# Kernel optimization log

Hardware: AMD Instinct MI355X
Metric: run time of the kernel (lower is better)

The kernel has to match this reference:

```python
import jax, jax.numpy as jnp
import numpy as np

B, C_IN, N, K = 8, 64, 16384, 9
C_OUT = 128


def setup_inputs() -> dict:
    key = jax.random.key(0)
    k1, k2, k3, k4 = jax.random.split(key, 4)
    x = jax.random.normal(k1, (B, C_IN, N, 1), dtype=jnp.float32)
    edge_index = jax.random.randint(k2, (2, B, N, K), 0, N, dtype=jnp.int32)
    # 1x1 Conv2d weight/bias of the MLP2dLayer: in = 2*C_IN, out = C_OUT
    W = jax.random.normal(k3, (C_OUT, 2 * C_IN), dtype=jnp.float32) * (1.0 / np.sqrt(2 * C_IN))
    b = jax.random.normal(k4, (C_OUT,), dtype=jnp.float32) * 0.01
    return {"x": x, "edge_index": edge_index, "W": W, "b": b}


def reference(x, edge_index, W, b):
    # x: [B, C, N, 1]; edge_index: [2, B, N, K] (edge_index[0] = neighbor idx)
    Bb, C, Nn, _ = x.shape
    idx = edge_index[0]                      # [B, N, K]
    x3 = x[..., 0]                           # [B, C, N]
    # batched_index_select: gather neighbor features x_j [B, C, N, K]
    idx_flat = idx.reshape(Bb, 1, Nn * idx.shape[-1])
    idx_flat = jnp.broadcast_to(idx_flat, (Bb, C, idx_flat.shape[-1]))
    x_j = jnp.take_along_axis(x3, idx_flat, axis=2).reshape(Bb, C, Nn, -1)
    # max-relative aggregation over neighbors (keepdim)
    aggr = jnp.max(x_j - x3[..., None], axis=-1, keepdims=True)  # [B, C, N, 1]
    feat = jnp.concatenate([x, aggr], axis=1)                    # [B, 2C, N, 1]
    # 1x1 conv MLP + ReLU (norm=None)
    out = jnp.einsum('oc,bcnk->bonk', W, feat) + b[None, :, None, None]
    return jax.nn.relu(out)
```

## Files before the change

kernel.cpp:

```cpp
#include <hip/hip_runtime.h>
#include <float.h>

#define NB 8
#define CIN 64
#define NPTS 16384
#define KNB 9
#define COUT 128
#define TN 64
#define FPAD 65
#define LDB 136

typedef float f32x4 __attribute__((ext_vector_type(4)));
typedef __bf16 bf16x8 __attribute__((ext_vector_type(8)));

__device__ __forceinline__ ushort f2bf_rne(float f) {
    unsigned u = __float_as_uint(f);
    unsigned r = u + 0x7FFFu + ((u >> 16) & 1u);
    return (ushort)(r >> 16);
}
__device__ __forceinline__ float bf2f(ushort h) {
    return __uint_as_float(((unsigned)h) << 16);
}

__global__ __launch_bounds__(256) void prep_kernel(const float* __restrict__ x,
                                                   const float* __restrict__ W,
                                                   float* __restrict__ xt,
                                                   ushort* __restrict__ Whi,
                                                   ushort* __restrict__ Wlo) {
    int blk = blockIdx.x;
    if (blk == NB * (NPTS / 64)) {
        for (int i = threadIdx.x; i < COUT * 2 * CIN; i += 256) {
            float w = W[i];
            ushort h = f2bf_rne(w);
            Whi[i] = h;
            Wlo[i] = f2bf_rne(w - bf2f(h));
        }
        return;
    }
    __shared__ float t[64][65];
    int b   = blk >> 8;
    int n0  = (blk & 255) << 6;
    int tid = threadIdx.x;
    int hi  = tid >> 4;
    int lo  = tid & 15;
    const float* xb = x + (size_t)b * CIN * NPTS;

#pragma unroll
    for (int cc = 0; cc < 4; ++cc) {
        int c = cc * 16 + hi;
        int n = lo * 4;
        float4 v = *reinterpret_cast<const float4*>(&xb[(size_t)c * NPTS + n0 + n]);
        t[c][n + 0] = v.x; t[c][n + 1] = v.y; t[c][n + 2] = v.z; t[c][n + 3] = v.w;
    }
    __syncthreads();

    float* xtb = xt + (size_t)b * NPTS * 64;
#pragma unroll
    for (int it = 0; it < 4; ++it) {
        int n  = it * 16 + hi;
        int c4 = lo * 4;
        float4 v;
        v.x = t[c4 + 0][n]; v.y = t[c4 + 1][n]; v.z = t[c4 + 2][n]; v.w = t[c4 + 3][n];
        *reinterpret_cast<float4*>(&xtb[(size_t)(n0 + n) * 64 + c4]) = v;
    }
}

__global__ __launch_bounds__(256, 4) void mrconv_main(const int*    __restrict__ eidx,
                                                      const ushort* __restrict__ Whi,
                                                      const ushort* __restrict__ Wlo,
                                                      const float*  __restrict__ bias,
                                                      const float*  __restrict__ xt,
                                                      float*        __restrict__ out) {
    __shared__ __align__(16) ushort fhi[TN][LDB];
    __shared__ __align__(16) ushort flo[TN][LDB];

    int blk  = blockIdx.x;
    int b    = blk & 7;
    int tile = blk >> 3;
    int n0   = tile * TN;

    int tid  = threadIdx.x;
    int lane = tid & 63;
    int wid  = __builtin_amdgcn_readfirstlane(tid >> 6);
    int l16  = lane & 15;
    int lh   = lane >> 4;

    const float* xtb = xt + (size_t)b * NPTS * 64;
    const int*   eb  = eidx + ((size_t)b * NPTS + n0) * KNB;

#pragma unroll 2
    for (int i = 0; i < 16; ++i) {
        int n = wid * 16 + i;
        float xc = xtb[(size_t)(n0 + n) * 64 + lane];
        ushort xh = f2bf_rne(xc);
        fhi[n][lane] = xh;
        flo[n][lane] = f2bf_rne(xc - bf2f(xh));
        const int* ep = eb + n * KNB;
        float m = -FLT_MAX;
#pragma unroll
        for (int k = 0; k < KNB; ++k) {
            int j = ep[k];
            float xj = xtb[(size_t)j * 64 + lane];
            m = fmaxf(m, xj - xc);
        }
        ushort mh = f2bf_rne(m);
        fhi[n][CIN + lane] = mh;
        flo[n][CIN + lane] = f2bf_rne(m - bf2f(mh));
    }

    bf16x8 ahi[2][4], alo[2][4];
#pragma unroll
    for (int mt = 0; mt < 2; ++mt)
#pragma unroll
        for (int kb = 0; kb < 4; ++kb) {
            int off = (wid * 32 + mt * 16 + l16) * (2 * CIN) + kb * 32 + lh * 8;
            ahi[mt][kb] = *reinterpret_cast<const bf16x8*>(Whi + off);
            alo[mt][kb] = *reinterpret_cast<const bf16x8*>(Wlo + off);
        }

    __syncthreads();

    f32x4 acc[2][4];
#pragma unroll
    for (int mt = 0; mt < 2; ++mt)
#pragma unroll
        for (int nt = 0; nt < 4; ++nt)
            acc[mt][nt] = (f32x4){0.f, 0.f, 0.f, 0.f};

#pragma unroll
    for (int nt = 0; nt < 4; ++nt) {
#pragma unroll
        for (int kb = 0; kb < 4; ++kb) {
            const bf16x8 bhi = *reinterpret_cast<const bf16x8*>(&fhi[nt * 16 + l16][kb * 32 + lh * 8]);
            const bf16x8 blo = *reinterpret_cast<const bf16x8*>(&flo[nt * 16 + l16][kb * 32 + lh * 8]);
#pragma unroll
            for (int mt = 0; mt < 2; ++mt) {
                acc[mt][nt] = __builtin_amdgcn_mfma_f32_16x16x32_bf16(ahi[mt][kb], bhi, acc[mt][nt], 0, 0, 0);
                acc[mt][nt] = __builtin_amdgcn_mfma_f32_16x16x32_bf16(ahi[mt][kb], blo, acc[mt][nt], 0, 0, 0);
                acc[mt][nt] = __builtin_amdgcn_mfma_f32_16x16x32_bf16(alo[mt][kb], bhi, acc[mt][nt], 0, 0, 0);
            }
        }
    }

    float* ob = out + (size_t)b * COUT * NPTS + n0;
#pragma unroll
    for (int mt = 0; mt < 2; ++mt)
#pragma unroll
        for (int nt = 0; nt < 4; ++nt)
#pragma unroll
            for (int r = 0; r < 4; ++r) {
                int o = wid * 32 + mt * 16 + lh * 4 + r;
                int n = nt * 16 + l16;
                float v = acc[mt][nt][r] + bias[o];
                ob[(size_t)o * NPTS + n] = fmaxf(v, 0.f);
            }
}

__global__ __launch_bounds__(256) void mrconv_direct(const float* __restrict__ x,
                                                     const int*   __restrict__ eidx,
                                                     const float* __restrict__ W,
                                                     const float* __restrict__ bias,
                                                     float* __restrict__ out) {
    __shared__ float feat[2 * CIN][FPAD];

    int blk  = blockIdx.x;
    int b    = blk & 7;
    int tile = blk >> 3;
    int n0   = tile * TN;

    int tid  = threadIdx.x;
    int lane = tid & 63;
    int wid  = __builtin_amdgcn_readfirstlane(tid >> 6);

    const float* xb = x + (size_t)b * CIN * NPTS;
    const int*   eb = eidx + ((size_t)b * NPTS + n0) * KNB;

#pragma unroll
    for (int i = 0; i < 16; ++i) {
        int c = wid * 16 + i;
        feat[c][lane] = xb[(size_t)c * NPTS + n0 + lane];
    }
    __syncthreads();

    const float* xc_row = xb + (size_t)lane * NPTS;
#pragma unroll 2
    for (int i = 0; i < 16; ++i) {
        int n = i * 4 + wid;
        float xc = feat[lane][n];
        const int* ep = eb + n * KNB;
        float m = -FLT_MAX;
#pragma unroll
        for (int k = 0; k < KNB; ++k) {
            int j = ep[k];
            m = fmaxf(m, xc_row[j] - xc);
        }
        feat[CIN + lane][n] = m;
    }
    __syncthreads();

    int o_base = wid * 32;
    float acc[32];
#pragma unroll
    for (int oo = 0; oo < 32; ++oo) acc[oo] = 0.f;

    for (int c = 0; c < 2 * CIN; ++c) {
        float f = feat[c][lane];
#pragma unroll
        for (int oo = 0; oo < 32; ++oo)
            acc[oo] = fmaf(W[(o_base + oo) * (2 * CIN) + c], f, acc[oo]);
    }

    float* ob = out + (size_t)b * COUT * NPTS + n0;
#pragma unroll
    for (int oo = 0; oo < 32; ++oo) {
        int o = o_base + oo;
        float v = acc[oo] + bias[o];
        ob[(size_t)o * NPTS + lane] = fmaxf(v, 0.f);
    }
}

extern "C" void kernel_launch(void* const* d_in, const int* in_sizes, int n_in,
                              void* d_out, int out_size, void* d_ws, size_t ws_size,
                              hipStream_t stream) {
    const float* x    = (const float*)d_in[0];
    const int*   eidx = (const int*)  d_in[1];
    const float* W    = (const float*)d_in[2];
    const float* bias = (const float*)d_in[3];
    float*       out  = (float*)d_out;

    const size_t xt_elems = (size_t)NB * NPTS * 64;
    const size_t need = xt_elems * sizeof(float) + (size_t)2 * 2 * CIN * COUT * sizeof(ushort);

    if (ws_size >= need) {
        float*  xt  = (float*)d_ws;
        ushort* Whi = (ushort*)(xt + xt_elems);
        ushort* Wlo = Whi + (size_t)2 * CIN * COUT;

        dim3 blkA(256), grdA(NB * (NPTS / 64) + 1);
        hipLaunchKernelGGL(prep_kernel, grdA, blkA, 0, stream, x, W, xt, Whi, Wlo);

        dim3 blkB(256), grdB(NB * (NPTS / TN));
        hipLaunchKernelGGL(mrconv_main, grdB, blkB, 0, stream, eidx, Whi, Wlo, bias, xt, out);
    } else {
        dim3 blkB(256), grdB(NB * (NPTS / TN));
        hipLaunchKernelGGL(mrconv_direct, grdB, blkB, 0, stream, x, eidx, W, bias, out);
    }
}
```

Baseline: 144.1 us.

## Swizzle feature LDS layout, prefetch center features, raise occupancy hint to 5

Replaces the padded LDS feature tiles with unpadded 128-wide rows using an XOR swizzle on 8-element chunks, so the bf16x8 MFMA operand reads avoid bank conflicts and the tiles use less LDS. All 16 center-point features are loaded into registers up front and written to LDS before the gather loop, which is now unrolled by 4 so more neighbor loads can be in flight. The launch bound goes from 4 to 5 blocks per SM. The tradeoff is higher register pressure under a tighter occupancy bound, which could cause spills.

```diff
diff --git a/kernel.cpp b/kernel.cpp
--- a/kernel.cpp
+++ b/kernel.cpp
@@ -8,7 +8,6 @@
 #define COUT 128
 #define TN 64
 #define FPAD 65
-#define LDB 136
 
 typedef float f32x4 __attribute__((ext_vector_type(4)));
 typedef __bf16 bf16x8 __attribute__((ext_vector_type(8)));
@@ -20,6 +19,10 @@
 }
 __device__ __forceinline__ float bf2f(ushort h) {
     return __uint_as_float(((unsigned)h) << 16);
+}
+
+__device__ __forceinline__ int swz16(int row, int us) {
+    return row * 128 + ((((us >> 3) ^ (row & 15)) << 3) | (us & 7));
 }
 
 __global__ __launch_bounds__(256) void prep_kernel(const float* __restrict__ x,
@@ -65,14 +68,14 @@
     }
 }
 
-__global__ __launch_bounds__(256, 4) void mrconv_main(const int*    __restrict__ eidx,
+__global__ __launch_bounds__(256, 5) void mrconv_main(const int*    __restrict__ eidx,
                                                       const ushort* __restrict__ Whi,
                                                       const ushort* __restrict__ Wlo,
                                                       const float*  __restrict__ bias,
                                                       const float*  __restrict__ xt,
                                                       float*        __restrict__ out) {
-    __shared__ __align__(16) ushort fhi[TN][LDB];
-    __shared__ __align__(16) ushort flo[TN][LDB];
+    __shared__ __align__(16) ushort fhi[TN * 128];
+    __shared__ __align__(16) ushort flo[TN * 128];
 
     int blk  = blockIdx.x;
     int b    = blk & 7;
@@ -88,13 +91,23 @@
     const float* xtb = xt + (size_t)b * NPTS * 64;
     const int*   eb  = eidx + ((size_t)b * NPTS + n0) * KNB;
 
-#pragma unroll 2
+    float xcv[16];
+#pragma unroll
+    for (int i = 0; i < 16; ++i)
+        xcv[i] = xtb[(size_t)(n0 + wid * 16 + i) * 64 + lane];
+
+#pragma unroll
     for (int i = 0; i < 16; ++i) {
         int n = wid * 16 + i;
-        float xc = xtb[(size_t)(n0 + n) * 64 + lane];
-        ushort xh = f2bf_rne(xc);
-        fhi[n][lane] = xh;
-        flo[n][lane] = f2bf_rne(xc - bf2f(xh));
+        ushort xh = f2bf_rne(xcv[i]);
+        fhi[swz16(n, lane)] = xh;
+        flo[swz16(n, lane)] = f2bf_rne(xcv[i] - bf2f(xh));
+    }
+
+#pragma unroll 4
+    for (int i = 0; i < 16; ++i) {
+        int n = wid * 16 + i;
+        float xc = xcv[i];
         const int* ep = eb + n * KNB;
         float m = -FLT_MAX;
 #pragma unroll
@@ -104,8 +117,8 @@
             m = fmaxf(m, xj - xc);
         }
         ushort mh = f2bf_rne(m);
-        fhi[n][CIN + lane] = mh;
-        flo[n][CIN + lane] = f2bf_rne(m - bf2f(mh));
+        fhi[swz16(n, CIN + lane)] = mh;
+        flo[swz16(n, CIN + lane)] = f2bf_rne(m - bf2f(mh));
     }
 
     bf16x8 ahi[2][4], alo[2][4];
@@ -131,8 +144,9 @@
     for (int nt = 0; nt < 4; ++nt) {
 #pragma unroll
         for (int kb = 0; kb < 4; ++kb) {
-            const bf16x8 bhi = *reinterpret_cast<const bf16x8*>(&fhi[nt * 16 + l16][kb * 32 + lh * 8]);
-            const bf16x8 blo = *reinterpret_cast<const bf16x8*>(&flo[nt * 16 + l16][kb * 32 + lh * 8]);
+            int row = nt * 16 + l16;
+            const bf16x8 bhi = *reinterpret_cast<const bf16x8*>(&fhi[swz16(row, kb * 32 + lh * 8)]);
+            const bf16x8 blo = *reinterpret_cast<const bf16x8*>(&flo[swz16(row, kb * 32 + lh * 8)]);
 #pragma unroll
             for (int mt = 0; mt < 2; ++mt) {
                 acc[mt][nt] = __builtin_amdgcn_mfma_f32_16x16x32_bf16(ahi[mt][kb], bhi, acc[mt][nt], 0, 0, 0);
```

Measured after the change: 155.8 us. 1.08x slower.
